# Kernel tuning notes

Measured on AMD Instinct MI355X. Metric: run time of the kernel, lower is better.

Reference implementation:

```python
import jax, jax.numpy as jnp
import numpy as np

NUM_HEADS = 16
DEPTH = 0


def rotate_half(x):
    x1, x2 = jnp.split(x, 2, axis=-1)
    return jnp.concatenate((-x2, x1), axis=-1)


def rotary_tables(seq_len, rot_dim, dtype):
    # RotaryEmbedding(dim=rot_dim): inv_freq over even indices of rot_dim
    inv_freq = 1.0 / (10000.0 ** (jnp.arange(0, rot_dim, 2, dtype=jnp.float32) / rot_dim))
    freqs = jnp.arange(seq_len, dtype=jnp.float32)[:, None] * inv_freq[None, :]  # [N, rot_dim/2]
    emb = jnp.concatenate((freqs, freqs), axis=-1)  # [N, rot_dim]
    return emb.astype(dtype), jnp.cos(emb).astype(dtype), jnp.sin(emb).astype(dtype)


def setup_inputs() -> dict:
    key = jax.random.key(0)
    ks = jax.random.split(key, 7)
    B, N, C = 1, 2048, 1024
    hd = C // NUM_HEADS
    std_qkv = (1.0 / C) ** 0.5
    std_proj = (1.0 / (2 * C)) ** 0.5
    return {
        "x": jax.random.normal(ks[0], (B, N, C), dtype=jnp.float32),
        "W_qkv": jax.random.normal(ks[1], (6 * C, C), dtype=jnp.float32) * std_qkv,
        "W_proj": jax.random.normal(ks[2], (C, 2 * C), dtype=jnp.float32) * std_proj,
        "lambda_q1": jax.random.normal(ks[3], (hd,), dtype=jnp.float32) * 0.1,
        "lambda_q2": jax.random.normal(ks[4], (hd,), dtype=jnp.float32) * 0.1,
        "lambda_k1": jax.random.normal(ks[5], (hd,), dtype=jnp.float32) * 0.1,
        "lambda_k2": jax.random.normal(ks[6], (hd,), dtype=jnp.float32) * 0.1,
    }


def reference(x, W_qkv, W_proj, lambda_q1, lambda_q2, lambda_k1, lambda_k2):
    B, N, C = x.shape
    H = NUM_HEADS
    hd = C // H
    scale = hd ** -0.5
    lambda_init = 0.8 - 0.6 * np.exp(-0.3 * DEPTH)

    qkv = jnp.einsum('bnc,dc->bnd', x, W_qkv)               # [B,N,6C]
    qkv = qkv.reshape(B, N, 6, H, hd).transpose(2, 0, 3, 1, 4)  # [6,B,H,N,hd]
    q = jnp.concatenate((qkv[0], qkv[1]), axis=-1)          # [B,H,N,2hd]
    k = jnp.concatenate((qkv[2], qkv[3]), axis=-1)
    v = jnp.concatenate((qkv[4], qkv[5]), axis=-1)

    _, cos, sin = rotary_tables(N, 2 * hd, x.dtype)          # [N,2hd]
    q = q * cos + rotate_half(q) * sin
    k = k * cos + rotate_half(k) * sin

    q1, q2 = jnp.split(q, 2, axis=-1)                        # [B,H,N,hd] each
    k1, k2 = jnp.split(k, 2, axis=-1)

    attn1 = jnp.einsum('bhid,bhjd->bhij', q1, k1) * scale
    attn2 = jnp.einsum('bhid,bhjd->bhij', q2, k2) * scale

    lam1 = jnp.exp(jnp.sum(lambda_q1 * lambda_k1))
    lam2 = jnp.exp(jnp.sum(lambda_q2 * lambda_k2))
    lam = (lam1 - lam2 + lambda_init).astype(x.dtype)

    probs = jax.nn.softmax(attn1, axis=-1) - lam * jax.nn.softmax(attn2, axis=-1)
    out = jnp.einsum('bhij,bhjd->bhid', probs, v)            # [B,H,N,2hd]
    out = out.transpose(0, 2, 1, 3).reshape(B, N, 2 * C)
    out = jnp.einsum('bnd,cd->bnc', out, W_proj)             # [B,N,C]
    return out
```

## Files before the change

kernel.cpp:

```cpp
#include <hip/hip_runtime.h>

using bf16_t = __bf16;
typedef __bf16 bf16x8 __attribute__((ext_vector_type(8)));
typedef float floatx4 __attribute__((ext_vector_type(4)));

#define MFMA_BF16(a, b, c) __builtin_amdgcn_mfma_f32_16x16x32_bf16((a), (b), (c), 0, 0, 0)

__device__ __forceinline__ void async_ld16(bf16_t* lds_dst, const bf16_t* g_src) {
    __builtin_amdgcn_global_load_lds(
        (const __attribute__((address_space(1))) void*)g_src,
        (__attribute__((address_space(3))) void*)lds_dst, 16, 0, 0);
}

__global__ __launch_bounds__(256) void cast_bf16(const float* __restrict__ src,
                                                 bf16_t* __restrict__ dst, int n8) {
    int i = blockIdx.x * 256 + threadIdx.x;
    if (i < n8) {
        const floatx4 a = *(const floatx4*)(src + (size_t)i * 8);
        const floatx4 b = *(const floatx4*)(src + (size_t)i * 8 + 4);
        bf16x8 r;
        r[0] = (bf16_t)a[0]; r[1] = (bf16_t)a[1]; r[2] = (bf16_t)a[2]; r[3] = (bf16_t)a[3];
        r[4] = (bf16_t)b[0]; r[5] = (bf16_t)b[1]; r[6] = (bf16_t)b[2]; r[7] = (bf16_t)b[3];
        *(bf16x8*)(dst + (size_t)i * 8) = r;
    }
}

__global__ void lam_kernel(const float* lq1, const float* lq2,
                           const float* lk1, const float* lk2, float* lamp) {
    int l = threadIdx.x;
    float p1 = lq1[l] * lk1[l];
    float p2 = lq2[l] * lk2[l];
    #pragma unroll
    for (int d = 1; d < 64; d <<= 1) {
        p1 += __shfl_xor(p1, d);
        p2 += __shfl_xor(p2, d);
    }
    if (l == 0) *lamp = expf(p1) - expf(p2) + 0.2f;
}

template <int BM, int BN, bool QKV_EPI, typename TC>
__global__ __launch_bounds__(256) void gemm_bt(const bf16_t* __restrict__ A,
                                               const bf16_t* __restrict__ B,
                                               TC* __restrict__ C,
                                               bf16_t* __restrict__ Qb,
                                               bf16_t* __restrict__ Kb,
                                               bf16_t* __restrict__ Vt,
                                               int M, int N, int K) {
    constexpr int BK = 32;
    __shared__ __align__(16) bf16_t As[BM * BK];
    __shared__ __align__(16) bf16_t Bs[BN * BK];
    const int t = threadIdx.x;
    const int lane = t & 63, wave = t >> 6;
    const int q4 = lane >> 4, m16 = lane & 15;
    const int mblk = blockIdx.y * BM, nblk = blockIdx.x * BN;
    const int wr = wave >> 1, wc = wave & 1;
    constexpr int WM = BM / 2, WN = BN / 2;
    constexpr int NI = WM / 16, NJ = WN / 16;
    constexpr int AR = BM * BK / 2048;
    constexpr int BR = BN * BK / 2048;

    floatx4 acc[NI][NJ] = {};

    for (int k0 = 0; k0 < K; k0 += BK) {
        __syncthreads();
        #pragma unroll
        for (int rr = 0; rr < AR; ++rr) {
            int f = rr * 256 + t;
            async_ld16(&As[f * 8], &A[(size_t)(mblk + (f >> 2)) * K + k0 + (f & 3) * 8]);
        }
        #pragma unroll
        for (int rr = 0; rr < BR; ++rr) {
            int f = rr * 256 + t;
            async_ld16(&Bs[f * 8], &B[(size_t)(nblk + (f >> 2)) * K + k0 + (f & 3) * 8]);
        }
        __syncthreads();

        bf16x8 a[NI], b[NJ];
        #pragma unroll
        for (int i = 0; i < NI; ++i)
            a[i] = *(const bf16x8*)&As[(wr * WM + i * 16 + m16) * 32 + q4 * 8];
        #pragma unroll
        for (int j = 0; j < NJ; ++j)
            b[j] = *(const bf16x8*)&Bs[(wc * WN + j * 16 + m16) * 32 + q4 * 8];
        #pragma unroll
        for (int i = 0; i < NI; ++i)
            #pragma unroll
            for (int j = 0; j < NJ; ++j)
                acc[i][j] = MFMA_BF16(a[i], b[j], acc[i][j]);
    }

    #pragma unroll
    for (int i = 0; i < NI; ++i)
        #pragma unroll
        for (int j = 0; j < NJ; ++j) {
            int n = nblk + wc * WN + j * 16 + m16;
            #pragma unroll
            for (int r = 0; r < 4; ++r) {
                int m = mblk + wr * WM + i * 16 + q4 * 4 + r;
                if constexpr (QKV_EPI) {
                    bf16_t val = (bf16_t)acc[i][j][r];
                    int comp = n >> 10, h = (n >> 6) & 15, e = n & 63;
                    if (comp < 2)
                        Qb[(size_t)((comp * 16 + h) * 2048 + m) * 64 + e] = val;
                    else if (comp < 4)
                        Kb[(size_t)(((comp - 2) * 16 + h) * 2048 + m) * 64 + e] = val;
                    else
                        Vt[(size_t)(h * 128 + (comp - 4) * 64 + e) * 2048 + m] = val;
                } else {
                    C[(size_t)m * N + n] = (TC)acc[i][j][r];
                }
            }
        }
}

__global__ __launch_bounds__(256) void rotary_inplace(bf16_t* __restrict__ Qb,
                                                      bf16_t* __restrict__ Kb) {
    int t = blockIdx.x * 256 + threadIdx.x;
    int e = t & 63, h = (t >> 6) & 15, n = t >> 10;
    float invf = exp2f(-(float)e * (13.287712379549449f / 64.0f));
    float ang = (float)n * invf;
    float s, c;
    sincosf(ang, &s, &c);
    int off = (h * 2048 + n) * 64 + e;
    float q1 = (float)Qb[off], q2 = (float)Qb[off + 2097152];
    Qb[off]           = (bf16_t)(q1 * c - q2 * s);
    Qb[off + 2097152] = (bf16_t)(q2 * c + q1 * s);
    float k1 = (float)Kb[off], k2 = (float)Kb[off + 2097152];
    Kb[off]           = (bf16_t)(k1 * c - k2 * s);
    Kb[off + 2097152] = (bf16_t)(k2 * c + k1 * s);
}

__global__ __launch_bounds__(256, 2) void flash_diff(const bf16_t* __restrict__ Qb,
                                                     const bf16_t* __restrict__ Kb,
                                                     const bf16_t* __restrict__ Vt,
                                                     const float* __restrict__ lamp,
                                                     bf16_t* __restrict__ Ao) {
    constexpr int N = 2048, BN = 64;
    __shared__ __align__(16) bf16_t Kf[16 * 512];
    __shared__ __align__(16) bf16_t Vf[16 * 512];
    __shared__ __align__(16) bf16_t Pf[4 * 2 * 1024];
    const int t = threadIdx.x, lane = t & 63, w = t >> 6;
    const int q4 = lane >> 4, m16 = lane & 15;
    const int h = blockIdx.y, qt = blockIdx.x;
    const float lam = *lamp;
    const float cexp = 0.125f * 1.4426950408889634f;
    const int mm = lane & 15, qq = lane >> 4;

    bf16x8 qf[2][2];
    const int qrow = qt * 64 + w * 16 + m16;
    #pragma unroll
    for (int i = 0; i < 2; ++i)
        #pragma unroll
        for (int kc = 0; kc < 2; ++kc)
            qf[i][kc] = *(const bf16x8*)&Qb[(size_t)((i * 16 + h) * 2048 + qrow) * 64 + kc * 32 + q4 * 8];

    bf16x8 ones;
    #pragma unroll
    for (int j = 0; j < 8; ++j) ones[j] = (bf16_t)1.0f;

    floatx4 O[2][8] = {};
    floatx4 sm[2] = {};

    for (int k0 = 0; k0 < N; k0 += BN) {
        __syncthreads();
        #pragma unroll
        for (int rr = 0; rr < 8; ++rr) {
            int idx = w * 8 + rr;
            if (idx < 16) {
                int i = idx >> 3, s = (idx >> 1) & 3, half = idx & 1;
                async_ld16(&Kf[idx * 512],
                           &Kb[(size_t)((i * 16 + h) * 2048 + k0 + 16 * s + mm) * 64 + half * 32 + qq * 8]);
            } else {
                int v = idx - 16, tt = v >> 1, half = v & 1;
                async_ld16(&Vf[v * 512],
                           &Vt[(size_t)(h * 128 + tt * 16 + mm) * 2048 + k0 + half * 32 + qq * 8]);
            }
        }
        __syncthreads();

        #pragma unroll
        for (int i = 0; i < 2; ++i) {
            #pragma unroll
            for (int s = 0; s < 4; ++s) {
                floatx4 sacc = {};
                const bf16x8 kf0 = *(const bf16x8*)&Kf[((i * 4 + s) * 2 + 0) * 512 + (q4 * 16 + m16) * 8];
                const bf16x8 kf1 = *(const bf16x8*)&Kf[((i * 4 + s) * 2 + 1) * 512 + (q4 * 16 + m16) * 8];
                sacc = MFMA_BF16(qf[i][0], kf0, sacc);
                sacc = MFMA_BF16(qf[i][1], kf1, sacc);
                const int half = s >> 1, quad = (2 * s + (m16 >> 3)) & 3, jj = m16 & 7;
                bf16_t* pb = &Pf[((w * 2 + i) * 2 + half) * 512 + quad * 128 + jj];
                #pragma unroll
                for (int r = 0; r < 4; ++r)
                    pb[(q4 * 4 + r) * 8] = (bf16_t)exp2f(sacc[r] * cexp);
            }
        }
        __syncthreads();

        bf16x8 pf[2][2];
        #pragma unroll
        for (int i = 0; i < 2; ++i) {
            pf[i][0] = *(const bf16x8*)&Pf[((w * 2 + i) * 2 + 0) * 512 + (q4 * 16 + m16) * 8];
            pf[i][1] = *(const bf16x8*)&Pf[((w * 2 + i) * 2 + 1) * 512 + (q4 * 16 + m16) * 8];
            sm[i] = MFMA_BF16(pf[i][0], ones, sm[i]);
            sm[i] = MFMA_BF16(pf[i][1], ones, sm[i]);
        }
        #pragma unroll
        for (int tt = 0; tt < 8; ++tt) {
            const bf16x8 vf0 = *(const bf16x8*)&Vf[(tt * 2 + 0) * 512 + (q4 * 16 + m16) * 8];
            const bf16x8 vf1 = *(const bf16x8*)&Vf[(tt * 2 + 1) * 512 + (q4 * 16 + m16) * 8];
            #pragma unroll
            for (int i = 0; i < 2; ++i) {
                O[i][tt] = MFMA_BF16(pf[i][0], vf0, O[i][tt]);
                O[i][tt] = MFMA_BF16(pf[i][1], vf1, O[i][tt]);
            }
        }
    }

    float inv0[4], inv1[4];
    #pragma unroll
    for (int r = 0; r < 4; ++r) {
        inv0[r] = 1.0f / sm[0][r];
        inv1[r] = 1.0f / sm[1][r];
    }
    const int orow = qt * 64 + w * 16;
    #pragma unroll
    for (int tt = 0; tt < 8; ++tt)
        #pragma unroll
        for (int r = 0; r < 4; ++r) {
            float val = O[0][tt][r] * inv0[r] - lam * O[1][tt][r] * inv1[r];
            Ao[(size_t)(orow + q4 * 4 + r) * 2048 + h * 128 + tt * 16 + m16] = (bf16_t)val;
        }
}

extern "C" void kernel_launch(void* const* d_in, const int* in_sizes, int n_in,
                              void* d_out, int out_size, void* d_ws, size_t ws_size,
                              hipStream_t stream) {
    const float* x     = (const float*)d_in[0];
    const float* Wqkv  = (const float*)d_in[1];
    const float* Wproj = (const float*)d_in[2];
    const float* lq1   = (const float*)d_in[3];
    const float* lq2   = (const float*)d_in[4];
    const float* lk1   = (const float*)d_in[5];
    const float* lk2   = (const float*)d_in[6];
    float* out = (float*)d_out;

    char* ws = (char*)d_ws;
    bf16_t* xb     = (bf16_t*)(ws);
    bf16_t* Ao     = (bf16_t*)(ws);
    bf16_t* Wqkvb  = (bf16_t*)(ws + 4194304);
    bf16_t* Wprojb = (bf16_t*)(ws + 16777216);
    bf16_t* Qb     = (bf16_t*)(ws + 20971520);
    bf16_t* Kb     = (bf16_t*)(ws + 29360128);
    bf16_t* Vt     = (bf16_t*)(ws + 37748736);
    float*  lamp   = (float*)(ws + 46137344);

    lam_kernel<<<1, 64, 0, stream>>>(lq1, lq2, lk1, lk2, lamp);
    cast_bf16<<<1024, 256, 0, stream>>>(x, xb, 2048 * 1024 / 8);
    cast_bf16<<<3072, 256, 0, stream>>>(Wqkv, Wqkvb, 6144 * 1024 / 8);
    cast_bf16<<<1024, 256, 0, stream>>>(Wproj, Wprojb, 1024 * 2048 / 8);
    gemm_bt<128, 128, true, float><<<dim3(48, 16), 256, 0, stream>>>(
        xb, Wqkvb, (float*)nullptr, Qb, Kb, Vt, 2048, 6144, 1024);
    rotary_inplace<<<(2048 * 16 * 64) / 256, 256, 0, stream>>>(Qb, Kb);
    flash_diff<<<dim3(32, 16), 256, 0, stream>>>(Qb, Kb, Vt, lamp, Ao);
    gemm_bt<128, 64, false, float><<<dim3(16, 16), 256, 0, stream>>>(
        Ao, Wprojb, out, (bf16_t*)nullptr, (bf16_t*)nullptr, (bf16_t*)nullptr,
        2048, 1024, 2048);
}
```

Baseline: 277.0 us.

## Split differential attention components across 8 waves with LDS combine and XOR-swizzled P

The flash_diff kernel now uses 512 threads per block. Waves 0-3 handle the first softmax component and waves 4-7 the second, instead of each wave computing both, and the two partial outputs are combined through LDS at the end. The P tile writes use an XOR swizzle to reduce LDS bank conflicts, and the middle barrier between the S and PV phases is removed because each wave only reads its own P slice. The block index is also remapped so that consecutive blocks spread across heads. This halves per-wave register state and raises parallelism, at the cost of an extra LDS round-trip and more threads sharing each K/V tile load.

```diff
diff --git a/kernel.cpp b/kernel.cpp
--- a/kernel.cpp
+++ b/kernel.cpp
@@ -130,106 +130,114 @@
     Kb[off + 2097152] = (bf16_t)(k2 * c + k1 * s);
 }
 
-__global__ __launch_bounds__(256, 2) void flash_diff(const bf16_t* __restrict__ Qb,
+__global__ __launch_bounds__(512, 4) void flash_diff(const bf16_t* __restrict__ Qb,
                                                      const bf16_t* __restrict__ Kb,
                                                      const bf16_t* __restrict__ Vt,
                                                      const float* __restrict__ lamp,
                                                      bf16_t* __restrict__ Ao) {
     constexpr int N = 2048, BN = 64;
-    __shared__ __align__(16) bf16_t Kf[16 * 512];
-    __shared__ __align__(16) bf16_t Vf[16 * 512];
-    __shared__ __align__(16) bf16_t Pf[4 * 2 * 1024];
+    __shared__ __align__(16) bf16_t smem[24576];
+    bf16_t* Kf = smem;
+    bf16_t* Vf = smem + 8192;
+    bf16_t* Pf = smem + 16384;
     const int t = threadIdx.x, lane = t & 63, w = t >> 6;
+    const int comp = w >> 2, w4 = w & 3;
     const int q4 = lane >> 4, m16 = lane & 15;
-    const int h = blockIdx.y, qt = blockIdx.x;
+    const int Lb = blockIdx.x;
+    const int virt = (Lb & 7) * 64 + (Lb >> 3);
+    const int h = virt >> 5, qt = virt & 31;
     const float lam = *lamp;
     const float cexp = 0.125f * 1.4426950408889634f;
-    const int mm = lane & 15, qq = lane >> 4;
-
-    bf16x8 qf[2][2];
-    const int qrow = qt * 64 + w * 16 + m16;
-    #pragma unroll
-    for (int i = 0; i < 2; ++i)
-        #pragma unroll
-        for (int kc = 0; kc < 2; ++kc)
-            qf[i][kc] = *(const bf16x8*)&Qb[(size_t)((i * 16 + h) * 2048 + qrow) * 64 + kc * 32 + q4 * 8];
+
+    bf16x8 qf[2];
+    const int qrow = qt * 64 + w4 * 16 + m16;
+    #pragma unroll
+    for (int kc = 0; kc < 2; ++kc)
+        qf[kc] = *(const bf16x8*)&Qb[(size_t)((comp * 16 + h) * 2048 + qrow) * 64 + kc * 32 + q4 * 8];
 
     bf16x8 ones;
     #pragma unroll
     for (int j = 0; j < 8; ++j) ones[j] = (bf16_t)1.0f;
 
-    floatx4 O[2][8] = {};
-    floatx4 sm[2] = {};
+    floatx4 O[8] = {};
+    floatx4 sm = {};
 
     for (int k0 = 0; k0 < N; k0 += BN) {
         __syncthreads();
         #pragma unroll
-        for (int rr = 0; rr < 8; ++rr) {
-            int idx = w * 8 + rr;
+        for (int rr = 0; rr < 4; ++rr) {
+            int idx = w * 4 + rr;
             if (idx < 16) {
                 int i = idx >> 3, s = (idx >> 1) & 3, half = idx & 1;
                 async_ld16(&Kf[idx * 512],
-                           &Kb[(size_t)((i * 16 + h) * 2048 + k0 + 16 * s + mm) * 64 + half * 32 + qq * 8]);
+                           &Kb[(size_t)((i * 16 + h) * 2048 + k0 + 16 * s + m16) * 64 + half * 32 + q4 * 8]);
             } else {
                 int v = idx - 16, tt = v >> 1, half = v & 1;
                 async_ld16(&Vf[v * 512],
-                           &Vt[(size_t)(h * 128 + tt * 16 + mm) * 2048 + k0 + half * 32 + qq * 8]);
-            }
-        }
-        __syncthreads();
-
-        #pragma unroll
-        for (int i = 0; i < 2; ++i) {
-            #pragma unroll
-            for (int s = 0; s < 4; ++s) {
-                floatx4 sacc = {};
-                const bf16x8 kf0 = *(const bf16x8*)&Kf[((i * 4 + s) * 2 + 0) * 512 + (q4 * 16 + m16) * 8];
-                const bf16x8 kf1 = *(const bf16x8*)&Kf[((i * 4 + s) * 2 + 1) * 512 + (q4 * 16 + m16) * 8];
-                sacc = MFMA_BF16(qf[i][0], kf0, sacc);
-                sacc = MFMA_BF16(qf[i][1], kf1, sacc);
-                const int half = s >> 1, quad = (2 * s + (m16 >> 3)) & 3, jj = m16 & 7;
-                bf16_t* pb = &Pf[((w * 2 + i) * 2 + half) * 512 + quad * 128 + jj];
-                #pragma unroll
-                for (int r = 0; r < 4; ++r)
-                    pb[(q4 * 4 + r) * 8] = (bf16_t)exp2f(sacc[r] * cexp);
-            }
-        }
-        __syncthreads();
-
-        bf16x8 pf[2][2];
-        #pragma unroll
-        for (int i = 0; i < 2; ++i) {
-            pf[i][0] = *(const bf16x8*)&Pf[((w * 2 + i) * 2 + 0) * 512 + (q4 * 16 + m16) * 8];
-            pf[i][1] = *(const bf16x8*)&Pf[((w * 2 + i) * 2 + 1) * 512 + (q4 * 16 + m16) * 8];
-            sm[i] = MFMA_BF16(pf[i][0], ones, sm[i]);
-            sm[i] = MFMA_BF16(pf[i][1], ones, sm[i]);
-        }
+                           &Vt[(size_t)(h * 128 + tt * 16 + m16) * 2048 + k0 + half * 32 + q4 * 8]);
+            }
+        }
+        __syncthreads();
+
+        bf16_t* pw = &Pf[w * 1024];
+        #pragma unroll
+        for (int s = 0; s < 4; ++s) {
+            floatx4 sacc = {};
+            const bf16x8 kf0 = *(const bf16x8*)&Kf[((comp * 4 + s) * 2 + 0) * 512 + lane * 8];
+            const bf16x8 kf1 = *(const bf16x8*)&Kf[((comp * 4 + s) * 2 + 1) * 512 + lane * 8];
+            sacc = MFMA_BF16(qf[0], kf0, sacc);
+            sacc = MFMA_BF16(qf[1], kf1, sacc);
+            const int half = s >> 1, quad = (2 * s + (m16 >> 3)) & 3, jj = m16 & 7;
+            #pragma unroll
+            for (int r = 0; r < 4; ++r) {
+                int u = quad * 16 + q4 * 4 + r;
+                pw[half * 512 + (u ^ quad) * 8 + jj] = (bf16_t)exp2f(sacc[r] * cexp);
+            }
+        }
+
+        bf16x8 pf[2];
+        const int ur = lane ^ q4;
+        pf[0] = *(const bf16x8*)&pw[0 * 512 + ur * 8];
+        pf[1] = *(const bf16x8*)&pw[1 * 512 + ur * 8];
+        sm = MFMA_BF16(pf[0], ones, sm);
+        sm = MFMA_BF16(pf[1], ones, sm);
         #pragma unroll
         for (int tt = 0; tt < 8; ++tt) {
-            const bf16x8 vf0 = *(const bf16x8*)&Vf[(tt * 2 + 0) * 512 + (q4 * 16 + m16) * 8];
-            const bf16x8 vf1 = *(const bf16x8*)&Vf[(tt * 2 + 1) * 512 + (q4 * 16 + m16) * 8];
-            #pragma unroll
-            for (int i = 0; i < 2; ++i) {
-                O[i][tt] = MFMA_BF16(pf[i][0], vf0, O[i][tt]);
-                O[i][tt] = MFMA_BF16(pf[i][1], vf1, O[i][tt]);
-            }
-        }
-    }
-
-    float inv0[4], inv1[4];
-    #pragma unroll
-    for (int r = 0; r < 4; ++r) {
-        inv0[r] = 1.0f / sm[0][r];
-        inv1[r] = 1.0f / sm[1][r];
-    }
-    const int orow = qt * 64 + w * 16;
-    #pragma unroll
-    for (int tt = 0; tt < 8; ++tt)
-        #pragma unroll
-        for (int r = 0; r < 4; ++r) {
-            float val = O[0][tt][r] * inv0[r] - lam * O[1][tt][r] * inv1[r];
-            Ao[(size_t)(orow + q4 * 4 + r) * 2048 + h * 128 + tt * 16 + m16] = (bf16_t)val;
-        }
+            const bf16x8 vf0 = *(const bf16x8*)&Vf[(tt * 2 + 0) * 512 + lane * 8];
+            const bf16x8 vf1 = *(const bf16x8*)&Vf[(tt * 2 + 1) * 512 + lane * 8];
+            O[tt] = MFMA_BF16(pf[0], vf0, O[tt]);
+            O[tt] = MFMA_BF16(pf[1], vf1, O[tt]);
+        }
+    }
+
+    float inv[4];
+    #pragma unroll
+    for (int r = 0; r < 4; ++r) inv[r] = 1.0f / sm[r];
+
+    float* Ff = (float*)smem;
+    __syncthreads();
+    if (comp == 1) {
+        #pragma unroll
+        for (int tt = 0; tt < 8; ++tt) {
+            floatx4 val;
+            #pragma unroll
+            for (int r = 0; r < 4; ++r) val[r] = lam * O[tt][r] * inv[r];
+            *(floatx4*)&Ff[((w4 * 128 + tt * 16 + m16) << 4) + q4 * 4] = val;
+        }
+    }
+    __syncthreads();
+    if (comp == 0) {
+        const int orow = qt * 64 + w4 * 16 + q4 * 4;
+        #pragma unroll
+        for (int tt = 0; tt < 8; ++tt) {
+            const floatx4 v1 = *(const floatx4*)&Ff[((w4 * 128 + tt * 16 + m16) << 4) + q4 * 4];
+            #pragma unroll
+            for (int r = 0; r < 4; ++r) {
+                float val = O[tt][r] * inv[r] - v1[r];
+                Ao[(size_t)(orow + r) * 2048 + h * 128 + tt * 16 + m16] = (bf16_t)val;
+            }
+        }
+    }
 }
 
 extern "C" void kernel_launch(void* const* d_in, const int* in_sizes, int n_in,
@@ -261,7 +269,7 @@
     gemm_bt<128, 128, true, float><<<dim3(48, 16), 256, 0, stream>>>(
         xb, Wqkvb, (float*)nullptr, Qb, Kb, Vt, 2048, 6144, 1024);
     rotary_inplace<<<(2048 * 16 * 64) / 256, 256, 0, stream>>>(Qb, Kb);
-    flash_diff<<<dim3(32, 16), 256, 0, stream>>>(Qb, Kb, Vt, lamp, Ao);
+    flash_diff<<<512, 512, 0, stream>>>(Qb, Kb, Vt, lamp, Ao);
     gemm_bt<128, 64, false, float><<<dim3(16, 16), 256, 0, stream>>>(
         Ao, Wprojb, out, (bf16_t*)nullptr, (bf16_t*)nullptr, (bf16_t*)nullptr,
         2048, 1024, 2048);
```

After: 265.9 us. -4.0%, faster.
